# Kernel optimization log

Measured on AMD Instinct MI355X. Metric: run time of the kernel, lower is better.

The kernel has to match this reference:

```python
import jax, jax.numpy as jnp
import numpy as np

H = 16      # numHeads (== numKeyValueHeads since keyValueHeadsPerHead=1)
D = 128     # headDim


def setup_inputs() -> dict:
    key = jax.random.key(0)
    k1, k2, k3 = jax.random.split(key, 3)
    B, S, dim = 2, 2048, 2048
    x = jax.random.normal(k1, (B, S, dim), dtype=jnp.float32)
    # qkvProj: Linear(dim -> (H + 2*H)*D) without bias; torch Linear weight is [out, in]
    Wqkv = jax.random.normal(k2, ((H + 2 * H) * D, dim), dtype=jnp.float32) * 0.02
    # outProj: Linear(H*D -> dim) without bias
    Wout = jax.random.normal(k3, (dim, H * D), dtype=jnp.float32) * 0.02
    return {"x": x, "Wqkv": Wqkv, "Wout": Wout}


def reference(x, Wqkv, Wout):
    B, S, _ = x.shape
    qkv = jnp.einsum('bsd,ed->bse', x, Wqkv)           # [B, S, 3*H*D]
    qkv = qkv.reshape(B, S, 3 * H, D)
    q = qkv[:, :, :H]                                  # [B, S, H, D]
    k = qkv[:, :, H:2 * H]                             # [B, S, H, D]
    v = qkv[:, :, 2 * H:]                              # [B, S, H, D]
    # explicit QK^T / sqrt(d), softmax in fp32, then @ V (keyValueHeadsPerHead=1
    # collapses the group axis, leaving standard per-head attention)
    logits = jnp.einsum('bqhd,bkhd->bhqk', q, k) * (D ** -0.5)
    w = jax.nn.softmax(logits.astype(jnp.float32), axis=-1).astype(logits.dtype)
    out = jnp.einsum('bhqk,bkhd->bqhd', w, v).reshape(B, S, H * D)
    return jnp.einsum('bse,de->bsd', out, Wout)        # outProj
```

## Files before the change

kernel.cpp:

```cpp
#include <hip/hip_runtime.h>

typedef __bf16 bf16x8 __attribute__((ext_vector_type(8)));
typedef _Float16 f16;
typedef f16 f16x8 __attribute__((ext_vector_type(8)));
typedef float f32x4 __attribute__((ext_vector_type(4)));
typedef unsigned short u16;
typedef u16 u16x4 __attribute__((ext_vector_type(4)));

__device__ __forceinline__ u16 f2bf(float f) {
  unsigned u = __builtin_bit_cast(unsigned, f);
  u += 0x7FFFu + ((u >> 16) & 1u);
  return (u16)(u >> 16);
}

#define GLDS16(g, l) __builtin_amdgcn_global_load_lds(                     \
    (const __attribute__((address_space(1))) unsigned int*)(g),            \
    (__attribute__((address_space(3))) unsigned int*)(l), 16, 0, 0)

__device__ __forceinline__ f32x4 mfma16(bf16x8 a, bf16x8 b, f32x4 c) {
  return __builtin_amdgcn_mfma_f32_16x16x32_bf16(a, b, c, 0, 0, 0);
}
__device__ __forceinline__ f32x4 mfma16h(f16x8 a, f16x8 b, f32x4 c) {
  return __builtin_amdgcn_mfma_f32_16x16x32_f16(a, b, c, 0, 0, 0);
}

__global__ void cvt_bf16(const float* __restrict__ src, u16* __restrict__ dst,
                         int n4, int n4s, float scale) {
  int idx = blockIdx.x * blockDim.x + threadIdx.x;
  int stride = gridDim.x * blockDim.x;
  for (int i = idx; i < n4; i += stride) {
    float4 v = ((const float4*)src)[i];
    float sc = (i < n4s) ? scale : 1.0f;
    u16x4 o = { f2bf(v.x * sc), f2bf(v.y * sc), f2bf(v.z * sc), f2bf(v.w * sc) };
    ((u16x4*)dst)[i] = o;
  }
}

__global__ __launch_bounds__(512, 2) void gemm1_qkv(
    const u16* __restrict__ A, const u16* __restrict__ B,
    u16* __restrict__ QK, u16* __restrict__ VT) {
  __shared__ __align__(16) u16 L[4][16384];
  constexpr int K = 2048;
  const int t = threadIdx.x, lane = t & 63, w = t >> 6;
  const int wm = w >> 2, wn = w & 3;
  const int l15 = lane & 15, lg = lane >> 4;

  const int bid = blockIdx.x;
  const int wg = (bid & 7) * 48 + (bid >> 3);
  const int bx = wg % 24, by = wg / 24;
  const int m0 = by * 256, n0 = bx * 256;

  const int csrc = ((t & 3) ^ ((t >> 2) & 3) ^ ((t >> 4) & 3)) * 8;
  const u16* ga = A + (size_t)(m0 + (t >> 2)) * K + csrc;
  const u16* gb = B + (size_t)(n0 + (t >> 2)) * K + csrc;
  const int rchunk = (lg ^ (l15 & 3) ^ (l15 >> 2)) * 8;

  f32x4 acc[8][4] = {};

#define STAGE1(kt, bf) do {                                                \
    u16* la_ = &L[bf][0]; u16* lb_ = &L[bf][8192];                         \
    const int ko_ = (kt) * 32;                                             \
    GLDS16(ga + ko_,           la_ + t * 8);                               \
    GLDS16(ga + ko_ + 128 * K, la_ + 4096 + t * 8);                        \
    GLDS16(gb + ko_,           lb_ + t * 8);                               \
    GLDS16(gb + ko_ + 128 * K, lb_ + 4096 + t * 8);                        \
  } while (0)

#define GBODY(kt, VM) do {                                                 \
    asm volatile("s_waitcnt vmcnt(" #VM ")" ::: "memory");                 \
    __builtin_amdgcn_sched_barrier(0);                                     \
    __builtin_amdgcn_s_barrier();                                          \
    __builtin_amdgcn_sched_barrier(0);                                     \
    const u16* la_ = &L[(kt) & 3][0];                                      \
    const u16* lb_ = &L[(kt) & 3][8192];                                   \
    bf16x8 af[8]; bf16x8 bfr[4];                                           \
    _Pragma("unroll")                                                      \
    for (int i_ = 0; i_ < 8; ++i_)                                         \
      af[i_] = *(const bf16x8*)&la_[(wm * 128 + i_ * 16 + l15) * 32 + rchunk]; \
    _Pragma("unroll")                                                      \
    for (int j_ = 0; j_ < 4; ++j_)                                         \
      bfr[j_] = *(const bf16x8*)&lb_[(wn * 64 + j_ * 16 + l15) * 32 + rchunk]; \
    __builtin_amdgcn_s_setprio(1);                                         \
    _Pragma("unroll")                                                      \
    for (int i_ = 0; i_ < 8; ++i_)                                         \
      _Pragma("unroll")                                                    \
      for (int j_ = 0; j_ < 4; ++j_)                                       \
        acc[i_][j_] = mfma16(af[i_], bfr[j_], acc[i_][j_]);                \
    __builtin_amdgcn_s_setprio(0);                                         \
    asm volatile("s_waitcnt lgkmcnt(0)" ::: "memory");                     \
    __builtin_amdgcn_sched_barrier(0);                                     \
    __builtin_amdgcn_s_barrier();                                          \
    __builtin_amdgcn_sched_barrier(0);                                     \
  } while (0)

  STAGE1(0, 0); STAGE1(1, 1); STAGE1(2, 2);
#pragma unroll 1
  for (int it = 0; it <= 60; ++it) {
    STAGE1(it + 3, (it + 3) & 3);
    GBODY(it, 12);
  }
  GBODY(61, 8);
  GBODY(62, 4);
  GBODY(63, 0);
#undef STAGE1
#undef GBODY

  const int rb = m0 + wm * 128 + lg * 4;
  const int cb0 = wn * 64 + l15;
  if (n0 < 4096) {
#pragma unroll
    for (int i = 0; i < 8; ++i)
#pragma unroll
      for (int j = 0; j < 4; ++j) {
        const int row0 = rb + i * 16;
        const int col = n0 + cb0 + j * 16;
#pragma unroll
        for (int jj = 0; jj < 4; ++jj)
          QK[(size_t)(row0 + jj) * 4096 + col] = f2bf(acc[i][j][jj]);
      }
  } else {
#pragma unroll
    for (int i = 0; i < 8; ++i)
#pragma unroll
      for (int j = 0; j < 4; ++j) {
        const int row0 = rb + i * 16;
        const int vcol = (n0 - 4096) + cb0 + j * 16;
        const int bb = row0 >> 11, s = row0 & 2047;
        auto h0 = __builtin_amdgcn_cvt_pkrtz(acc[i][j][0], acc[i][j][1]);
        auto h1 = __builtin_amdgcn_cvt_pkrtz(acc[i][j][2], acc[i][j][3]);
        uint2 pk;
        pk.x = __builtin_bit_cast(unsigned, h0);
        pk.y = __builtin_bit_cast(unsigned, h1);
        *(uint2*)&VT[((size_t)bb * 2048 + vcol) * 2048 + s] = pk;
      }
  }
}

__global__ __launch_bounds__(256, 2) void gemm_bt(
    const u16* __restrict__ A, const u16* __restrict__ B,
    float* __restrict__ C, int M, int N, int K) {
  __shared__ __align__(16) u16 As[128 * 32];
  __shared__ __align__(16) u16 Bs[128 * 32];
  const int t = threadIdx.x;
  const int lane = t & 63;
  const int w = t >> 6;
  const int wm = w >> 1, wn = w & 1;
  const int m0 = blockIdx.y * 128, n0 = blockIdx.x * 128;
  f32x4 acc[4][4] = {};

  const u16* ga = A + (size_t)(m0 + (t >> 2)) * K + (t & 3) * 8;
  const u16* gb = B + (size_t)(n0 + (t >> 2)) * K + (t & 3) * 8;
  u16* la = (u16*)As + t * 8;
  u16* lb = (u16*)Bs + t * 8;
  const size_t half = (size_t)64 * K;

  for (int k0 = 0; k0 < K; k0 += 32) {
    GLDS16(ga + k0, la);
    GLDS16(ga + half + k0, la + 2048);
    GLDS16(gb + k0, lb);
    GLDS16(gb + half + k0, lb + 2048);
    __syncthreads();
    const int ro = (lane & 15) * 32 + (lane >> 4) * 8;
    bf16x8 af[4], bfr[4];
#pragma unroll
    for (int i = 0; i < 4; ++i) af[i]  = *(const bf16x8*)&As[(wm * 64 + i * 16) * 32 + ro];
#pragma unroll
    for (int i = 0; i < 4; ++i) bfr[i] = *(const bf16x8*)&Bs[(wn * 64 + i * 16) * 32 + ro];
#pragma unroll
    for (int i = 0; i < 4; ++i)
#pragma unroll
      for (int j = 0; j < 4; ++j)
        acc[i][j] = mfma16(af[i], bfr[j], acc[i][j]);
    __syncthreads();
  }

  const int rbase = m0 + wm * 64 + ((lane >> 4) << 2);
  const int cbase = n0 + wn * 64 + (lane & 15);
#pragma unroll
  for (int i = 0; i < 4; ++i)
#pragma unroll
    for (int j = 0; j < 4; ++j) {
      const int row0 = rbase + i * 16;
      const int col = cbase + j * 16;
#pragma unroll
      for (int jj = 0; jj < 4; ++jj)
        C[(size_t)(row0 + jj) * N + col] = acc[i][j][jj];
    }
}

#define PSTRIDE 72
__global__ __launch_bounds__(512, 1) void attn_fwd(
    const u16* __restrict__ qk, const u16* __restrict__ vt, u16* __restrict__ aout) {
  __shared__ __align__(16) u16 Ks[2][64 * 128];
  __shared__ __align__(16) u16 Vs[2][128 * 64];
  __shared__ __align__(16) u16 Pl[8][32 * PSTRIDE];
  const int t = threadIdx.x, lane = t & 63, w = t >> 6;
  const int bh = blockIdx.x;
  const int b = bh >> 4, h = bh & 15;
  const int q0 = blockIdx.y * 256 + w * 32;
  const int l15 = lane & 15, lg = lane >> 4;

  const u16* qp = qk + (size_t)b * 2048 * 4096 + h * 128;
  const u16* kp = qp + 2048;
  const u16* vtp = vt + (size_t)(b * 16 + h) * 128 * 2048;
  u16* op = aout + (size_t)b * 2048 * 2048 + h * 128;

  int ksoff[2], vsoff[2];
#pragma unroll
  for (int rd = 0; rd < 2; ++rd) {
    const int r = rd * 32 + (t >> 4);
    const int c = (t & 15) ^ (r & 15);
    ksoff[rd] = r * 4096 + c * 8;
    const int rv = rd * 64 + (t >> 3);
    const int cv = (t & 7) ^ (rv & 7);
    vsoff[rd] = rv * 2048 + cv * 8;
  }

  bf16x8 qf[2][4];
#pragma unroll
  for (int mi = 0; mi < 2; ++mi)
#pragma unroll
    for (int kd = 0; kd < 4; ++kd)
      qf[mi][kd] = *(const bf16x8*)&qp[(size_t)(q0 + mi * 16 + l15) * 4096 + kd * 32 + lg * 8];

  f32x4 o[2][8] = {};
  f32x4 lacc[2] = {};
  const f16x8 onesf = {f16(1.f), f16(1.f), f16(1.f), f16(1.f),
                       f16(1.f), f16(1.f), f16(1.f), f16(1.f)};
  u16* pw = &Pl[w][0];

#pragma unroll
  for (int rd = 0; rd < 2; ++rd) {
    GLDS16(kp + ksoff[rd], &Ks[0][0] + rd * 4096 + t * 8);
    GLDS16(vtp + vsoff[rd], &Vs[0][0] + rd * 4096 + t * 8);
  }
  __syncthreads();

  auto tile = [&](const u16* ksb, const u16* vsb, u16* kpre, u16* vpre, int nextit) {
    if (nextit < 32) {
      const size_t kt1 = (size_t)nextit * 64;
#pragma unroll
      for (int rd = 0; rd < 2; ++rd) {
        GLDS16(kp + kt1 * 4096 + ksoff[rd], kpre + rd * 4096 + t * 8);
        GLDS16(vtp + kt1 + vsoff[rd], vpre + rd * 4096 + t * 8);
      }
    }
    f32x4 sf[2][4];
    __builtin_amdgcn_s_setprio(1);
#pragma unroll
    for (int ni = 0; ni < 4; ++ni) {
      const int r = ni * 16 + l15;
      bf16x8 kf[4];
#pragma unroll
      for (int kd = 0; kd < 4; ++kd)
        kf[kd] = *(const bf16x8*)&ksb[r * 128 + (((kd * 4 + lg) ^ l15) * 8)];
#pragma unroll
      for (int mi = 0; mi < 2; ++mi) {
        f32x4 s = {0.f, 0.f, 0.f, 0.f};
        s = mfma16(kf[0], qf[mi][0], s);
        s = mfma16(kf[1], qf[mi][1], s);
        s = mfma16(kf[2], qf[mi][2], s);
        s = mfma16(kf[3], qf[mi][3], s);
        sf[mi][ni] = s;
      }
    }
    __builtin_amdgcn_s_setprio(0);

#pragma unroll
    for (int mi = 0; mi < 2; ++mi)
#pragma unroll
      for (int ni = 0; ni < 4; ++ni) {
        float p0 = exp2f(sf[mi][ni][0]);
        float p1 = exp2f(sf[mi][ni][1]);
        float p2 = exp2f(sf[mi][ni][2]);
        float p3 = exp2f(sf[mi][ni][3]);
        auto h0 = __builtin_amdgcn_cvt_pkrtz(p0, p1);
        auto h1 = __builtin_amdgcn_cvt_pkrtz(p2, p3);
        uint2 wv;
        wv.x = __builtin_bit_cast(unsigned, h0);
        wv.y = __builtin_bit_cast(unsigned, h1);
        *(uint2*)&pw[(mi * 16 + l15) * PSTRIDE + ni * 16 + lg * 4] = wv;
      }

    f16x8 pa[2][2];
#pragma unroll
    for (int mi = 0; mi < 2; ++mi)
#pragma unroll
      for (int ks = 0; ks < 2; ++ks)
        pa[mi][ks] = *(const f16x8*)&pw[(mi * 16 + l15) * PSTRIDE + ks * 32 + lg * 8];
    __builtin_amdgcn_s_setprio(1);
#pragma unroll
    for (int mi = 0; mi < 2; ++mi) {
      lacc[mi] = mfma16h(pa[mi][0], onesf, lacc[mi]);
      lacc[mi] = mfma16h(pa[mi][1], onesf, lacc[mi]);
    }
#pragma unroll
    for (int n2 = 0; n2 < 8; ++n2) {
      const int r = n2 * 16 + l15;
      f16x8 vf0 = *(const f16x8*)&vsb[r * 64 + (((0 * 4 + lg) ^ (l15 & 7)) * 8)];
      f16x8 vf1 = *(const f16x8*)&vsb[r * 64 + (((1 * 4 + lg) ^ (l15 & 7)) * 8)];
#pragma unroll
      for (int mi = 0; mi < 2; ++mi) {
        o[mi][n2] = mfma16h(pa[mi][0], vf0, o[mi][n2]);
        o[mi][n2] = mfma16h(pa[mi][1], vf1, o[mi][n2]);
      }
    }
    __builtin_amdgcn_s_setprio(0);
    __syncthreads();
  };

#pragma unroll 1
  for (int it = 0; it < 32; it += 2) {
    tile(&Ks[0][0], &Vs[0][0], &Ks[1][0], &Vs[1][0], it + 1);
    tile(&Ks[1][0], &Vs[1][0], &Ks[0][0], &Vs[0][0], it + 2);
  }

#pragma unroll
  for (int mi = 0; mi < 2; ++mi)
#pragma unroll
    for (int j = 0; j < 4; ++j) {
      float inv = 1.f / lacc[mi][j];
#pragma unroll
      for (int n2 = 0; n2 < 8; ++n2)
        op[(size_t)(q0 + mi * 16 + lg * 4 + j) * 2048 + n2 * 16 + l15] =
            f2bf(o[mi][n2][j] * inv);
    }
}

extern "C" void kernel_launch(void* const* d_in, const int* in_sizes, int n_in,
                              void* d_out, int out_size, void* d_ws, size_t ws_size,
                              hipStream_t stream) {
  const float* x    = (const float*)d_in[0];
  const float* Wqkv = (const float*)d_in[1];
  const float* Wout = (const float*)d_in[2];
  float* out = (float*)d_out;

  u16* ws = (u16*)d_ws;
  u16* xb    = ws;
  u16* wqkvb = ws + 8388608;
  u16* woutb = ws + 20971520;
  u16* qkbuf = ws + 25165824;
  u16* vtbuf = ws + 41943040;
  u16* aout  = xb;

  const float qscale = 0.08838834764831845f * 1.4426950408889634f;

  cvt_bf16<<<2048, 256, 0, stream>>>(x,    xb,    8388608 / 4, 0, 1.0f);
  cvt_bf16<<<2048, 256, 0, stream>>>(Wqkv, wqkvb, 12582912 / 4, 4194304 / 4, qscale);
  cvt_bf16<<<1024, 256, 0, stream>>>(Wout, woutb, 4194304 / 4, 0, 1.0f);

  gemm1_qkv<<<384, 512, 0, stream>>>(xb, wqkvb, qkbuf, vtbuf);
  attn_fwd<<<dim3(32, 8, 1), 512, 0, stream>>>(qkbuf, vtbuf, aout);
  gemm_bt<<<dim3(16, 32), 256, 0, stream>>>(aout, woutb, out, 4096, 2048, 2048);
}
```

Baseline: 286.2 us.

## Retile QKV GEMM to 128x384 blocks with double buffering and higher occupancy

The QKV projection GEMM moves from 256x256 tiles with a 4-deep LDS pipeline to 128x384 tiles with 2-deep buffering. The grid grows to 512 workgroups and launch bounds target 4 blocks per CU, so the launch covers all CUs more evenly and latency is hidden by occupancy rather than prefetch depth. The XOR swizzle on LDS reads is dropped, which may bring back bank conflicts, and each tile now does less arithmetic per byte loaded. Tiles can straddle the QK/V boundary, so the epilogue checks each column.

```diff
diff --git a/kernel.cpp b/kernel.cpp
--- a/kernel.cpp
+++ b/kernel.cpp
@@ -36,55 +36,53 @@
   }
 }
 
-__global__ __launch_bounds__(512, 2) void gemm1_qkv(
+__global__ __launch_bounds__(512, 4) void gemm1_qkv(
     const u16* __restrict__ A, const u16* __restrict__ B,
     u16* __restrict__ QK, u16* __restrict__ VT) {
-  __shared__ __align__(16) u16 L[4][16384];
+  __shared__ __align__(16) u16 L[2][16384];
   constexpr int K = 2048;
   const int t = threadIdx.x, lane = t & 63, w = t >> 6;
   const int wm = w >> 2, wn = w & 3;
   const int l15 = lane & 15, lg = lane >> 4;
 
   const int bid = blockIdx.x;
-  const int wg = (bid & 7) * 48 + (bid >> 3);
-  const int bx = wg % 24, by = wg / 24;
-  const int m0 = by * 256, n0 = bx * 256;
-
-  const int csrc = ((t & 3) ^ ((t >> 2) & 3) ^ ((t >> 4) & 3)) * 8;
-  const u16* ga = A + (size_t)(m0 + (t >> 2)) * K + csrc;
-  const u16* gb = B + (size_t)(n0 + (t >> 2)) * K + csrc;
-  const int rchunk = (lg ^ (l15 & 3) ^ (l15 >> 2)) * 8;
-
-  f32x4 acc[8][4] = {};
-
-#define STAGE1(kt, bf) do {                                                \
-    u16* la_ = &L[bf][0]; u16* lb_ = &L[bf][8192];                         \
+  const int wg = (bid & 7) * 64 + (bid >> 3);
+  const int bx = wg >> 5, by = wg & 31;
+  const int m0 = by * 128, n0 = bx * 384;
+
+  const u16* ga = A + (size_t)(m0 + (t >> 2)) * K + (t & 3) * 8;
+  const u16* gb = B + (size_t)(n0 + (t >> 2)) * K + (t & 3) * 8;
+
+  f32x4 acc[4][6] = {};
+
+#define STG(kt, bf) do {                                                   \
     const int ko_ = (kt) * 32;                                             \
-    GLDS16(ga + ko_,           la_ + t * 8);                               \
-    GLDS16(ga + ko_ + 128 * K, la_ + 4096 + t * 8);                        \
-    GLDS16(gb + ko_,           lb_ + t * 8);                               \
-    GLDS16(gb + ko_ + 128 * K, lb_ + 4096 + t * 8);                        \
+    u16* lp_ = &L[bf][0];                                                  \
+    GLDS16(ga + ko_,           lp_ + t * 8);                               \
+    GLDS16(gb + ko_,           lp_ + 4096 + t * 8);                        \
+    GLDS16(gb + ko_ + 128 * K, lp_ + 8192 + t * 8);                        \
+    GLDS16(gb + ko_ + 256 * K, lp_ + 12288 + t * 8);                       \
   } while (0)
 
-#define GBODY(kt, VM) do {                                                 \
+#define BODY(bf, VM) do {                                                  \
     asm volatile("s_waitcnt vmcnt(" #VM ")" ::: "memory");                 \
     __builtin_amdgcn_sched_barrier(0);                                     \
     __builtin_amdgcn_s_barrier();                                          \
     __builtin_amdgcn_sched_barrier(0);                                     \
-    const u16* la_ = &L[(kt) & 3][0];                                      \
-    const u16* lb_ = &L[(kt) & 3][8192];                                   \
-    bf16x8 af[8]; bf16x8 bfr[4];                                           \
+    const u16* la_ = &L[bf][0];                                            \
+    const u16* lb_ = &L[bf][4096];                                         \
+    bf16x8 af[4]; bf16x8 bfr[6];                                           \
     _Pragma("unroll")                                                      \
-    for (int i_ = 0; i_ < 8; ++i_)                                         \
-      af[i_] = *(const bf16x8*)&la_[(wm * 128 + i_ * 16 + l15) * 32 + rchunk]; \
+    for (int i_ = 0; i_ < 4; ++i_)                                         \
+      af[i_] = *(const bf16x8*)&la_[(wm * 64 + i_ * 16 + l15) * 32 + lg * 8]; \
     _Pragma("unroll")                                                      \
-    for (int j_ = 0; j_ < 4; ++j_)                                         \
-      bfr[j_] = *(const bf16x8*)&lb_[(wn * 64 + j_ * 16 + l15) * 32 + rchunk]; \
+    for (int j_ = 0; j_ < 6; ++j_)                                         \
+      bfr[j_] = *(const bf16x8*)&lb_[(wn * 96 + j_ * 16 + l15) * 32 + lg * 8]; \
     __builtin_amdgcn_s_setprio(1);                                         \
     _Pragma("unroll")                                                      \
-    for (int i_ = 0; i_ < 8; ++i_)                                         \
+    for (int i_ = 0; i_ < 4; ++i_)                                         \
       _Pragma("unroll")                                                    \
-      for (int j_ = 0; j_ < 4; ++j_)                                       \
+      for (int j_ = 0; j_ < 6; ++j_)                                       \
         acc[i_][j_] = mfma16(af[i_], bfr[j_], acc[i_][j_]);                \
     __builtin_amdgcn_s_setprio(0);                                         \
     asm volatile("s_waitcnt lgkmcnt(0)" ::: "memory");                     \
@@ -93,38 +91,30 @@
     __builtin_amdgcn_sched_barrier(0);                                     \
   } while (0)
 
-  STAGE1(0, 0); STAGE1(1, 1); STAGE1(2, 2);
+  STG(0, 0);
 #pragma unroll 1
-  for (int it = 0; it <= 60; ++it) {
-    STAGE1(it + 3, (it + 3) & 3);
-    GBODY(it, 12);
-  }
-  GBODY(61, 8);
-  GBODY(62, 4);
-  GBODY(63, 0);
-#undef STAGE1
-#undef GBODY
-
-  const int rb = m0 + wm * 128 + lg * 4;
-  const int cb0 = wn * 64 + l15;
-  if (n0 < 4096) {
-#pragma unroll
-    for (int i = 0; i < 8; ++i)
-#pragma unroll
-      for (int j = 0; j < 4; ++j) {
-        const int row0 = rb + i * 16;
-        const int col = n0 + cb0 + j * 16;
+  for (int it = 0; it < 63; ++it) {
+    STG(it + 1, (it + 1) & 1);
+    BODY(it & 1, 4);
+  }
+  BODY(1, 0);
+#undef STG
+#undef BODY
+
+  const int rb = m0 + wm * 64 + lg * 4;
+  const int cb = n0 + wn * 96 + l15;
+#pragma unroll
+  for (int i = 0; i < 4; ++i) {
+#pragma unroll
+    for (int j = 0; j < 6; ++j) {
+      const int row0 = rb + i * 16;
+      const int col = cb + j * 16;
+      if (col < 4096) {
 #pragma unroll
         for (int jj = 0; jj < 4; ++jj)
           QK[(size_t)(row0 + jj) * 4096 + col] = f2bf(acc[i][j][jj]);
-      }
-  } else {
-#pragma unroll
-    for (int i = 0; i < 8; ++i)
-#pragma unroll
-      for (int j = 0; j < 4; ++j) {
-        const int row0 = rb + i * 16;
-        const int vcol = (n0 - 4096) + cb0 + j * 16;
+      } else {
+        const int vcol = col - 4096;
         const int bb = row0 >> 11, s = row0 & 2047;
         auto h0 = __builtin_amdgcn_cvt_pkrtz(acc[i][j][0], acc[i][j][1]);
         auto h1 = __builtin_amdgcn_cvt_pkrtz(acc[i][j][2], acc[i][j][3]);
@@ -133,6 +123,7 @@
         pk.y = __builtin_bit_cast(unsigned, h1);
         *(uint2*)&VT[((size_t)bb * 2048 + vcol) * 2048 + s] = pk;
       }
+    }
   }
 }
 
@@ -349,7 +340,7 @@
   cvt_bf16<<<2048, 256, 0, stream>>>(Wqkv, wqkvb, 12582912 / 4, 4194304 / 4, qscale);
   cvt_bf16<<<1024, 256, 0, stream>>>(Wout, woutb, 4194304 / 4, 0, 1.0f);
 
-  gemm1_qkv<<<384, 512, 0, stream>>>(xb, wqkvb, qkbuf, vtbuf);
+  gemm1_qkv<<<512, 512, 0, stream>>>(xb, wqkvb, qkbuf, vtbuf);
   attn_fwd<<<dim3(32, 8, 1), 512, 0, stream>>>(qkbuf, vtbuf, aout);
   gemm_bt<<<dim3(16, 32), 256, 0, stream>>>(aout, woutb, out, 4096, 2048, 2048);
 }
```

Result: slower. 601.0 us (+110.0%).

## Restructure QKV GEMM mainloop into double-buffered K=64 tiles with quadrant-split compute

Applied to the files above, without the earlier changes.

Replaces the 4-stage K=32 LDS ring in the QKV projection GEMM with a 2-buffer K=64 scheme and an XOR swizzle over 8 chunks. Each iteration issues the next tile's loads in two halves, interleaved with four quadrant MFMA phases separated by barriers. The aim is fewer barrier/wait rounds per unit of K, with global loads hidden behind compute. In exchange it drops launch bounds to one workgroup per CU, which cuts occupancy, and adds more barriers per iteration.

```diff
diff --git a/kernel.cpp b/kernel.cpp
--- a/kernel.cpp
+++ b/kernel.cpp
@@ -36,74 +36,132 @@
   }
 }
 
-__global__ __launch_bounds__(512, 2) void gemm1_qkv(
+__global__ __launch_bounds__(512, 1) void gemm1_qkv(
     const u16* __restrict__ A, const u16* __restrict__ B,
     u16* __restrict__ QK, u16* __restrict__ VT) {
-  __shared__ __align__(16) u16 L[4][16384];
+  __shared__ __align__(16) u16 LA[2][16384];
+  __shared__ __align__(16) u16 LB[2][16384];
   constexpr int K = 2048;
   const int t = threadIdx.x, lane = t & 63, w = t >> 6;
   const int wm = w >> 2, wn = w & 3;
   const int l15 = lane & 15, lg = lane >> 4;
+  const int l7 = l15 & 7;
 
   const int bid = blockIdx.x;
   const int wg = (bid & 7) * 48 + (bid >> 3);
   const int bx = wg % 24, by = wg / 24;
   const int m0 = by * 256, n0 = bx * 256;
 
-  const int csrc = ((t & 3) ^ ((t >> 2) & 3) ^ ((t >> 4) & 3)) * 8;
-  const u16* ga = A + (size_t)(m0 + (t >> 2)) * K + csrc;
-  const u16* gb = B + (size_t)(n0 + (t >> 2)) * K + csrc;
-  const int rchunk = (lg ^ (l15 & 3) ^ (l15 >> 2)) * 8;
+  const int srow = t >> 3;
+  const int schunk = (t & 7) ^ (srow & 7);
+  const u16* ga = A + (size_t)(m0 + srow) * K + schunk * 8;
+  const u16* gb = B + (size_t)(n0 + srow) * K + schunk * 8;
 
   f32x4 acc[8][4] = {};
 
-#define STAGE1(kt, bf) do {                                                \
-    u16* la_ = &L[bf][0]; u16* lb_ = &L[bf][8192];                         \
-    const int ko_ = (kt) * 32;                                             \
-    GLDS16(ga + ko_,           la_ + t * 8);                               \
-    GLDS16(ga + ko_ + 128 * K, la_ + 4096 + t * 8);                        \
-    GLDS16(gb + ko_,           lb_ + t * 8);                               \
-    GLDS16(gb + ko_ + 128 * K, lb_ + 4096 + t * 8);                        \
+#define STG_HALF0(kt, bf) do {                                             \
+    const int ko_ = (kt) * 64;                                             \
+    GLDS16(ga + ko_,            &LA[bf][0]    + t * 8);                    \
+    GLDS16(ga + ko_ + 64  * K,  &LA[bf][4096] + t * 8);                    \
+    GLDS16(gb + ko_,            &LB[bf][0]    + t * 8);                    \
+    GLDS16(gb + ko_ + 64  * K,  &LB[bf][4096] + t * 8);                    \
   } while (0)
-
-#define GBODY(kt, VM) do {                                                 \
-    asm volatile("s_waitcnt vmcnt(" #VM ")" ::: "memory");                 \
-    __builtin_amdgcn_sched_barrier(0);                                     \
-    __builtin_amdgcn_s_barrier();                                          \
-    __builtin_amdgcn_sched_barrier(0);                                     \
-    const u16* la_ = &L[(kt) & 3][0];                                      \
-    const u16* lb_ = &L[(kt) & 3][8192];                                   \
-    bf16x8 af[8]; bf16x8 bfr[4];                                           \
-    _Pragma("unroll")                                                      \
-    for (int i_ = 0; i_ < 8; ++i_)                                         \
-      af[i_] = *(const bf16x8*)&la_[(wm * 128 + i_ * 16 + l15) * 32 + rchunk]; \
-    _Pragma("unroll")                                                      \
-    for (int j_ = 0; j_ < 4; ++j_)                                         \
-      bfr[j_] = *(const bf16x8*)&lb_[(wn * 64 + j_ * 16 + l15) * 32 + rchunk]; \
-    __builtin_amdgcn_s_setprio(1);                                         \
-    _Pragma("unroll")                                                      \
-    for (int i_ = 0; i_ < 8; ++i_)                                         \
-      _Pragma("unroll")                                                    \
-      for (int j_ = 0; j_ < 4; ++j_)                                       \
-        acc[i_][j_] = mfma16(af[i_], bfr[j_], acc[i_][j_]);                \
-    __builtin_amdgcn_s_setprio(0);                                         \
-    asm volatile("s_waitcnt lgkmcnt(0)" ::: "memory");                     \
-    __builtin_amdgcn_sched_barrier(0);                                     \
-    __builtin_amdgcn_s_barrier();                                          \
-    __builtin_amdgcn_sched_barrier(0);                                     \
+#define STG_HALF1(kt, bf) do {                                             \
+    const int ko_ = (kt) * 64;                                             \
+    GLDS16(ga + ko_ + 128 * K,  &LA[bf][8192]  + t * 8);                   \
+    GLDS16(ga + ko_ + 192 * K,  &LA[bf][12288] + t * 8);                   \
+    GLDS16(gb + ko_ + 128 * K,  &LB[bf][8192]  + t * 8);                   \
+    GLDS16(gb + ko_ + 192 * K,  &LB[bf][12288] + t * 8);                   \
   } while (0)
-
-  STAGE1(0, 0); STAGE1(1, 1); STAGE1(2, 2);
+#define BAR() do { __builtin_amdgcn_s_barrier();                           \
+                   __builtin_amdgcn_sched_barrier(0); } while (0)
+
+  STG_HALF0(0, 0); STG_HALF1(0, 0);
+  asm volatile("s_waitcnt vmcnt(0)" ::: "memory");
+  BAR();
+
 #pragma unroll 1
-  for (int it = 0; it <= 60; ++it) {
-    STAGE1(it + 3, (it + 3) & 3);
-    GBODY(it, 12);
-  }
-  GBODY(61, 8);
-  GBODY(62, 4);
-  GBODY(63, 0);
-#undef STAGE1
-#undef GBODY
+  for (int T = 0; T < 32; ++T) {
+    const int bf = T & 1, nbf = bf ^ 1;
+    const bool st = (T < 31);
+    const u16* la = &LA[bf][0];
+    const u16* lb = &LB[bf][0];
+    bf16x8 aF[2][4], bF0[2][2], bF1[2][2];
+
+    if (st) STG_HALF0(T + 1, nbf);
+#pragma unroll
+    for (int kk = 0; kk < 2; ++kk) {
+      const int cp = ((kk * 4 + lg) ^ l7) * 8;
+#pragma unroll
+      for (int i = 0; i < 4; ++i)
+        aF[kk][i] = *(const bf16x8*)&la[(wm * 128 + i * 16 + l15) * 64 + cp];
+#pragma unroll
+      for (int j = 0; j < 2; ++j)
+        bF0[kk][j] = *(const bf16x8*)&lb[(wn * 64 + j * 16 + l15) * 64 + cp];
+    }
+    __builtin_amdgcn_s_setprio(1);
+#pragma unroll
+    for (int i = 0; i < 4; ++i)
+#pragma unroll
+      for (int j = 0; j < 2; ++j)
+#pragma unroll
+        for (int kk = 0; kk < 2; ++kk)
+          acc[i][j] = mfma16(aF[kk][i], bF0[kk][j], acc[i][j]);
+    __builtin_amdgcn_s_setprio(0);
+    BAR();
+
+    if (st) STG_HALF1(T + 1, nbf);
+#pragma unroll
+    for (int kk = 0; kk < 2; ++kk) {
+      const int cp = ((kk * 4 + lg) ^ l7) * 8;
+#pragma unroll
+      for (int j = 0; j < 2; ++j)
+        bF1[kk][j] = *(const bf16x8*)&lb[(wn * 64 + 32 + j * 16 + l15) * 64 + cp];
+    }
+    __builtin_amdgcn_s_setprio(1);
+#pragma unroll
+    for (int i = 0; i < 4; ++i)
+#pragma unroll
+      for (int j = 0; j < 2; ++j)
+#pragma unroll
+        for (int kk = 0; kk < 2; ++kk)
+          acc[i][2 + j] = mfma16(aF[kk][i], bF1[kk][j], acc[i][2 + j]);
+    __builtin_amdgcn_s_setprio(0);
+    BAR();
+
+#pragma unroll
+    for (int kk = 0; kk < 2; ++kk) {
+      const int cp = ((kk * 4 + lg) ^ l7) * 8;
+#pragma unroll
+      for (int i = 0; i < 4; ++i)
+        aF[kk][i] = *(const bf16x8*)&la[(wm * 128 + 64 + i * 16 + l15) * 64 + cp];
+    }
+    __builtin_amdgcn_s_setprio(1);
+#pragma unroll
+    for (int i = 0; i < 4; ++i)
+#pragma unroll
+      for (int j = 0; j < 2; ++j)
+#pragma unroll
+        for (int kk = 0; kk < 2; ++kk)
+          acc[4 + i][j] = mfma16(aF[kk][i], bF0[kk][j], acc[4 + i][j]);
+    __builtin_amdgcn_s_setprio(0);
+    BAR();
+
+    __builtin_amdgcn_s_setprio(1);
+#pragma unroll
+    for (int i = 0; i < 4; ++i)
+#pragma unroll
+      for (int j = 0; j < 2; ++j)
+#pragma unroll
+        for (int kk = 0; kk < 2; ++kk)
+          acc[4 + i][2 + j] = mfma16(aF[kk][i], bF1[kk][j], acc[4 + i][2 + j]);
+    __builtin_amdgcn_s_setprio(0);
+    asm volatile("s_waitcnt vmcnt(0)" ::: "memory");
+    BAR();
+  }
+#undef STG_HALF0
+#undef STG_HALF1
+#undef BAR
 
   const int rb = m0 + wm * 128 + lg * 4;
   const int cb0 = wn * 64 + l15;
```

Measured after the change: 305.0 us. 6.6% more time.
